# Kernel tuning notes

Measured on AMD Instinct MI355X. Metric: run time of the kernel, lower is better.

Reference implementation:

```python
import jax, jax.numpy as jnp
import numpy as np

P = 8.0  # Lp norm order for NormDist layers (finite-p distance conv)
CHUNK = 8  # output-channel chunk for memory-bounded distance computation
EPS = 8.0 / 255.0


def lp_norm(d, p=P):
    # stable Lp norm over last axis: m * (sum((d/m)^p))^(1/p)
    m = jnp.max(d, axis=-1)
    ms = jnp.where(m > 0, m, 1.0)
    s = jnp.sum((d / ms[..., None]) ** p, axis=-1)
    ss = jnp.where(m > 0, s, 1.0)
    return m * ss ** (1.0 / p)


def extract_patches(t, k, s, pad):
    # [B,C,H,W] -> [B, L, C*k*k] (torch-unfold channel-major ordering), L=Ho*Wo
    pt = jax.lax.conv_general_dilated_patches(t, (k, k), (s, s), [(pad, pad), (pad, pad)])
    B, F, Ho, Wo = pt.shape
    return pt.reshape(B, F, Ho * Wo).transpose(0, 2, 1), Ho, Wo


def normdist_conv(c, lo, hi, w, k, s, pad):
    # Lp-distance conv with interval bound propagation on (center, lower, upper)
    pc, Ho, Wo = extract_patches(c, k, s, pad)
    pl, _, _ = extract_patches(lo, k, s, pad)
    ph, _, _ = extract_patches(hi, k, s, pad)
    O = w.shape[0]
    wf = w.reshape(O, -1)  # [O, F]

    def per_chunk(wc):  # wc: [CHUNK, F]
        dc = jnp.abs(pc[:, :, None, :] - wc)                     # [B,L,CHUNK,F]
        oc = lp_norm(dc)
        # per-element distance bounds given lo <= x <= hi
        dl = jnp.maximum(jnp.maximum(pl[:, :, None, :] - wc, wc - ph[:, :, None, :]), 0.0)
        ol = lp_norm(dl)
        dh = jnp.maximum(jnp.abs(pl[:, :, None, :] - wc), jnp.abs(ph[:, :, None, :] - wc))
        oh = lp_norm(dh)
        return oc, ol, oh

    oc, ol, oh = jax.lax.map(per_chunk, wf.reshape(O // CHUNK, CHUNK, -1))

    def to_img(t):  # [nch, B, L, CHUNK] -> [B, O, Ho, Wo]
        nch, B, L, ch = t.shape
        return t.transpose(1, 0, 3, 2).reshape(B, nch * ch, Ho, Wo)

    return to_img(oc), to_img(ol), to_img(oh)


def bound_relu(c, lo, hi):
    return jax.nn.relu(c), jax.nn.relu(lo), jax.nn.relu(hi)


def _mp(t):
    return jax.lax.reduce_window(t, -jnp.inf, jax.lax.max, (1, 1, 3, 3), (1, 1, 2, 2), 'VALID')


def bound_maxpool(c, lo, hi):
    return _mp(c), _mp(lo), _mp(hi)


def bound_linear(c, lo, hi, W, b=None):
    oc = c @ W.T
    mid = ((lo + hi) * 0.5) @ W.T
    rad = ((hi - lo) * 0.5) @ jnp.abs(W).T
    if b is not None:
        oc = oc + b
        mid = mid + b
    return oc, mid - rad, mid + rad


def setup_inputs() -> dict:
    key = jax.random.key(0)
    ks = jax.random.split(key, 10)
    x = jax.random.normal(ks[0], (16, 3, 32, 32), jnp.float32)
    lower = x - EPS
    upper = x + EPS
    w1 = jax.random.normal(ks[1], (96, 3, 7, 7), jnp.float32)
    w2 = jax.random.normal(ks[2], (256, 96, 5, 5), jnp.float32)
    w3 = jax.random.normal(ks[3], (384, 256, 3, 3), jnp.float32)
    w4 = jax.random.normal(ks[4], (384, 384, 3, 3), jnp.float32)
    w5 = jax.random.normal(ks[5], (256, 384, 3, 3), jnp.float32)
    fw1 = jax.random.normal(ks[6], (1024, 2304), jnp.float32) * 0.02
    fw2 = jax.random.normal(ks[7], (512, 1024), jnp.float32) * 0.03
    fw3 = jax.random.normal(ks[8], (10, 512), jnp.float32) * 0.04
    fb3 = jax.random.normal(ks[9], (10,), jnp.float32)
    return {"x": x, "lower": lower, "upper": upper, "w1": w1, "w2": w2, "w3": w3,
            "w4": w4, "w5": w5, "fw1": fw1, "fw2": fw2, "fw3": fw3, "fb3": fb3}


def reference(x, lower, upper, w1, w2, w3, w4, w5, fw1, fw2, fw3, fb3):
    c, l, u = normdist_conv(x, lower, upper, w1, 7, 2, 2)   # 32 -> 15
    c, l, u = bound_relu(c, l, u)
    c, l, u = bound_maxpool(c, l, u)                        # 15 -> 7
    c, l, u = normdist_conv(c, l, u, w2, 5, 1, 2)           # 7 -> 7
    c, l, u = bound_relu(c, l, u)
    c, l, u = bound_maxpool(c, l, u)                        # 7 -> 3
    c, l, u = normdist_conv(c, l, u, w3, 3, 1, 1)
    c, l, u = bound_relu(c, l, u)
    c, l, u = normdist_conv(c, l, u, w4, 3, 1, 1)
    c, l, u = bound_relu(c, l, u)
    c, l, u = normdist_conv(c, l, u, w5, 3, 1, 1)
    c, l, u = bound_relu(c, l, u)
    B = c.shape[0]
    c, l, u = c.reshape(B, -1), l.reshape(B, -1), u.reshape(B, -1)
    c, l, u = bound_linear(c, l, u, fw1)
    c, l, u = bound_relu(c, l, u)
    c, l, u = bound_linear(c, l, u, fw2)
    c, l, u = bound_relu(c, l, u)
    c, l, u = bound_linear(c, l, u, fw3, fb3)
    # final negation swaps the roles of lower/upper
    return (-c, -u, -l)
```

## Files before the change

### kernel.cpp

```cpp
#include <hip/hip_runtime.h>
#include <math.h>


__device__ __forceinline__ float rt8(float s) { return sqrtf(sqrtf(sqrtf(s))); }

__device__ __forceinline__ void tap16(float w, float pc, float pl, float pu,
                                      float& aC, float& aL, float& aH)
{
    float a = pc - w; float a2 = a * a, a4 = a2 * a2; aC = fmaf(a4, a4, aC);
    float x = pl - w, y = pu - w;
    float dl = fmaxf(fmaxf(x, -y), 0.f);
    float e2 = dl * dl, e4 = e2 * e2; aL = fmaf(e4, e4, aL);
    float h2 = fmaxf(x * x, y * y);
    float h4 = h2 * h2; aH = fmaf(h4, h4, aH);
}

template<int K, int S, int PAD, int CC, int HIN, int WIN, int HO, int WO, bool ROOT>
__launch_bounds__(256)
__global__ void conv_a(const float* __restrict__ IC, const float* __restrict__ IL,
                       const float* __restrict__ IU, const float* __restrict__ W,
                       float* __restrict__ OUT, int B, int Cin, int O, int OG)
{
    constexpr int PH = (HO - 1) * S + K;
    constexpr int PW = (WO - 1) * S + K;
    constexpr int PP = PH * PW;
    constexpr int HW = HIN * WIN;
    constexpr int NP = HO * WO;
    constexpr int ROUNDS = (NP + 63) / 64;
    __shared__ float lds[CC * 3 * PP];

    int og = blockIdx.x % OG;
    int b  = (blockIdx.x / OG) % B;
    int chunk = blockIdx.x / (OG * B);
    int c0 = chunk * CC;
    int tid = threadIdx.x;

    for (int i = tid; i < CC * 3 * PP; i += 256) lds[i] = 0.f;
    __syncthreads();
    for (int tsel = 0; tsel < 3; ++tsel) {
        const float* src = (tsel == 0 ? IC : (tsel == 1 ? IL : IU))
                         + ((size_t)b * Cin + c0) * HW;
        for (int e = tid; e < CC * HW; e += 256) {
            int c = e / HW, p = e % HW;
            int pr = p / WIN, pw_ = p % WIN;
            lds[c * 3 * PP + tsel * PP + (pr + PAD) * PW + (pw_ + PAD)] = src[e];
        }
    }
    __syncthreads();

    int wave = tid >> 6, lane = tid & 63;
    int o = __builtin_amdgcn_readfirstlane(og * 4 + wave);
    const float* wp = W + ((size_t)o * Cin + c0) * (K * K);

    for (int r = 0; r < ROUNDS; ++r) {
        int pos = r * 64 + lane;
        bool act = pos < NP;
        int pp = act ? pos : 0;
        int oh = pp / WO, ow = pp % WO;
        const float* sl = lds + (oh * S) * PW + ow * S;
        const float* wc = wp;
        float aC = 0.f, aL = 0.f, aH = 0.f;
        for (int c = 0; c < CC; ++c) {
            #pragma unroll
            for (int kh = 0; kh < K; ++kh)
                #pragma unroll
                for (int kw = 0; kw < K; ++kw) {
                    float w = wc[kh * K + kw];
                    tap16(w, sl[kh * PW + kw], sl[PP + kh * PW + kw],
                          sl[2 * PP + kh * PW + kw], aC, aL, aH);
                }
            sl += 3 * PP; wc += K * K;
        }
        if (act) {
            size_t N = (size_t)B * O * NP;
            size_t oidx = ((size_t)b * O + o) * NP + pos;
            if (ROOT) {
                OUT[oidx] = rt8(aC); OUT[N + oidx] = rt8(aL); OUT[2 * N + oidx] = rt8(aH);
            } else {
                float* P = OUT + (size_t)chunk * 3 * N;
                P[oidx] = aC; P[N + oidx] = aL; P[2 * N + oidx] = aH;
            }
        }
    }
}

template<int CC>
__launch_bounds__(128)
__global__ void conv2_kernel(const float* __restrict__ IN, const float* __restrict__ W,
                             float* __restrict__ P, int nin)
{
    constexpr int B = 16, Cin = 96, O = 256;
    __shared__ float slab[CC * 165];
    int x = blockIdx.x;
    int pair = x % 2;
    int oh   = (x / 2) % 7;
    int b    = (x / 14) % B;
    int chunk = x / (14 * B);
    int c0 = chunk * CC;
    int tid = threadIdx.x;

    for (int i = tid; i < CC * 165; i += 128) {
        int c = i / 165; int rem = i % 165;
        int tsel = rem / 55; int rr = rem % 55;
        int r = rr / 11, col = rr % 11;
        int ih = oh + r - 2, iw = col - 2;
        float v = 0.f;
        if ((unsigned)ih < 7u && (unsigned)iw < 7u)
            v = IN[(size_t)tsel * nin + ((size_t)b * Cin + c0 + c) * 49 + ih * 7 + iw];
        slab[i] = v;
    }
    __syncthreads();

    int wave = tid >> 6, lane = tid & 63;
    int o = (pair * 2 + wave) * 64 + lane;

    float aC[7], aL[7], aH[7];
    #pragma unroll
    for (int u = 0; u < 7; ++u) { aC[u] = 0.f; aL[u] = 0.f; aH[u] = 0.f; }

    for (int c = 0; c < CC; ++c) {
        const float* wp = W + ((size_t)o * Cin + c0 + c) * 25;
        float w[25];
        #pragma unroll
        for (int t = 0; t < 25; ++t) w[t] = wp[t];
        const float* sb = slab + c * 165;
        #pragma unroll
        for (int r = 0; r < 5; ++r) {
            #pragma unroll
            for (int i = 0; i < 11; ++i) {
                float xc = sb[r * 11 + i];
                float xl = sb[55 + r * 11 + i];
                float xu = sb[110 + r * 11 + i];
                #pragma unroll
                for (int ow = 0; ow < 7; ++ow) {
                    int kw = i - ow;
                    if (kw >= 0 && kw < 5)
                        tap16(w[r * 5 + kw], xc, xl, xu, aC[ow], aL[ow], aH[ow]);
                }
            }
        }
    }

    size_t N = (size_t)B * O * 49;
    size_t base = (((size_t)b * O + o) * 7 + oh) * 7;
    float* Pc = P + (size_t)chunk * 3 * N;
    #pragma unroll
    for (int u = 0; u < 7; ++u) {
        Pc[base + u] = aC[u]; Pc[N + base + u] = aL[u]; Pc[2 * N + base + u] = aH[u];
    }
}

template<int CC>
__launch_bounds__(128)
__global__ void conv3x3_kernel(const float* __restrict__ IN, const float* __restrict__ W,
                               float* __restrict__ P, int nin, int B, int Cin, int O,
                               int PAIRS)
{
    __shared__ float slab[CC * 75];
    int x = blockIdx.x;
    int pair = x % PAIRS;
    int b    = (x / PAIRS) % B;
    int chunk = x / (PAIRS * B);
    int c0 = chunk * CC;
    int tid = threadIdx.x;

    for (int i = tid; i < CC * 75; i += 128) {
        int c = i / 75; int rem = i % 75;
        int tsel = rem / 25; int rr = rem % 25;
        int iy = rr / 5, ix = rr % 5;
        int ih = iy - 1, iw = ix - 1;
        float v = 0.f;
        if ((unsigned)ih < 3u && (unsigned)iw < 3u)
            v = IN[(size_t)tsel * nin + ((size_t)b * Cin + c0 + c) * 9 + ih * 3 + iw];
        slab[i] = v;
    }
    __syncthreads();

    int wave = tid >> 6, lane = tid & 63;
    int o = (pair * 2 + wave) * 64 + lane;

    float aC[9], aL[9], aH[9];
    #pragma unroll
    for (int u = 0; u < 9; ++u) { aC[u] = 0.f; aL[u] = 0.f; aH[u] = 0.f; }

    for (int c = 0; c < CC; ++c) {
        const float* wp = W + ((size_t)o * Cin + c0 + c) * 9;
        float w[9];
        #pragma unroll
        for (int t = 0; t < 9; ++t) w[t] = wp[t];
        const float* sb = slab + c * 75;
        #pragma unroll
        for (int iy = 0; iy < 5; ++iy) {
            #pragma unroll
            for (int ix = 0; ix < 5; ++ix) {
                float xc = sb[iy * 5 + ix];
                float xl = sb[25 + iy * 5 + ix];
                float xu = sb[50 + iy * 5 + ix];
                #pragma unroll
                for (int py = 0; py < 3; ++py) {
                    int ky = iy - py;
                    if (ky < 0 || ky > 2) continue;
                    #pragma unroll
                    for (int px = 0; px < 3; ++px) {
                        int kx = ix - px;
                        if (kx < 0 || kx > 2) continue;
                        tap16(w[ky * 3 + kx], xc, xl, xu,
                              aC[py * 3 + px], aL[py * 3 + px], aH[py * 3 + px]);
                    }
                }
            }
        }
    }

    size_t N = (size_t)B * O * 9;
    size_t base = ((size_t)b * O + o) * 9;
    float* Pc = P + (size_t)chunk * 3 * N;
    #pragma unroll
    for (int u = 0; u < 9; ++u) {
        Pc[base + u] = aC[u]; Pc[N + base + u] = aL[u]; Pc[2 * N + base + u] = aH[u];
    }
}

__global__ void conv_combine(const float* __restrict__ P, float* __restrict__ OUT,
                             size_t N, int NCH)
{
    size_t idx = (size_t)blockIdx.x * blockDim.x + threadIdx.x;
    if (idx >= 3 * N) return;
    float s = 0.f;
    for (int ch = 0; ch < NCH; ++ch) s += P[(size_t)ch * 3 * N + idx];
    OUT[idx] = rt8(s);
}

__global__ void maxpool_kernel(const float* __restrict__ in, float* __restrict__ out,
                               int BC, int Hin, int Win, int Ho, int Wo,
                               int n_in, int n_out)
{
    int idx = blockIdx.x * blockDim.x + threadIdx.x;
    int per = BC * Ho * Wo;
    if (idx >= 3 * per) return;
    int tsel = idx / per; int r = idx - tsel * per;
    int ow = r % Wo; int t2 = r / Wo;
    int oh = t2 % Ho; int bc = t2 / Ho;
    const float* ip = in + (size_t)tsel * n_in + (size_t)bc * Hin * Win;
    int ih0 = oh * 2, iw0 = ow * 2;
    float m = -INFINITY;
    #pragma unroll
    for (int i = 0; i < 3; ++i)
        #pragma unroll
        for (int j = 0; j < 3; ++j)
            m = fmaxf(m, ip[(ih0 + i) * Win + (iw0 + j)]);
    out[(size_t)tsel * n_out + r] = m;
}

__global__ void fc_partial(
    const float* __restrict__ IC, const float* __restrict__ IL, const float* __restrict__ IU,
    const float* __restrict__ W, float* __restrict__ P,
    int B, int In, int Out, int CC, int NCH)
{
    int idx = blockIdx.x * blockDim.x + threadIdx.x;
    if (idx >= NCH * B * Out) return;
    int o = idx % Out; int t = idx / Out;
    int b = t % B; int chunk = t / B;
    int i0 = chunk * CC;
    const float4* wr = (const float4*)(W  + (size_t)o * In + i0);
    const float4* cr = (const float4*)(IC + (size_t)b * In + i0);
    const float4* lr = (const float4*)(IL + (size_t)b * In + i0);
    const float4* ur = (const float4*)(IU + (size_t)b * In + i0);
    float sc = 0.f, sm = 0.f, sr = 0.f;
    for (int i = 0; i < CC / 4; ++i) {
        float4 w4 = wr[i], c4 = cr[i], l4 = lr[i], u4 = ur[i];
        sc = fmaf(c4.x, w4.x, sc); sc = fmaf(c4.y, w4.y, sc);
        sc = fmaf(c4.z, w4.z, sc); sc = fmaf(c4.w, w4.w, sc);
        sm = fmaf((l4.x + u4.x) * 0.5f, w4.x, sm);
        sm = fmaf((l4.y + u4.y) * 0.5f, w4.y, sm);
        sm = fmaf((l4.z + u4.z) * 0.5f, w4.z, sm);
        sm = fmaf((l4.w + u4.w) * 0.5f, w4.w, sm);
        sr = fmaf((u4.x - l4.x) * 0.5f, fabsf(w4.x), sr);
        sr = fmaf((u4.y - l4.y) * 0.5f, fabsf(w4.y), sr);
        sr = fmaf((u4.z - l4.z) * 0.5f, fabsf(w4.z), sr);
        sr = fmaf((u4.w - l4.w) * 0.5f, fabsf(w4.w), sr);
    }
    size_t N = (size_t)B * Out;
    size_t base = (size_t)b * Out + o;
    float* p = P + (size_t)chunk * 3 * N;
    p[base] = sc; p[N + base] = sm; p[2 * N + base] = sr;
}

__global__ void fc_combine(const float* __restrict__ P, float* __restrict__ OUT,
                           size_t N, int NCH)
{
    size_t idx = (size_t)blockIdx.x * blockDim.x + threadIdx.x;
    if (idx >= N) return;
    float sc = 0.f, sm = 0.f, sr = 0.f;
    for (int ch = 0; ch < NCH; ++ch) {
        const float* p = P + (size_t)ch * 3 * N;
        sc += p[idx]; sm += p[N + idx]; sr += p[2 * N + idx];
    }
    OUT[idx]         = fmaxf(sc, 0.f);
    OUT[N + idx]     = fmaxf(sm - sr, 0.f);
    OUT[2 * N + idx] = fmaxf(sm + sr, 0.f);
}

__global__ void bound_linear_kernel(
    const float* __restrict__ IC, const float* __restrict__ IL, const float* __restrict__ IU,
    const float* __restrict__ W, const float* __restrict__ bias,
    float* __restrict__ OC, float* __restrict__ OL, float* __restrict__ OU,
    int B, int In, int Out)
{
    int idx = blockIdx.x * blockDim.x + threadIdx.x;
    if (idx >= B * Out) return;
    int o = idx % Out, b = idx / Out;
    const float* wr = W  + (size_t)o * In;
    const float* cr = IC + (size_t)b * In;
    const float* lr = IL + (size_t)b * In;
    const float* ur = IU + (size_t)b * In;
    float sc = 0.f, sm = 0.f, sr = 0.f;
    for (int i = 0; i < In; ++i) {
        float w = wr[i];
        sc = fmaf(cr[i], w, sc);
        sm = fmaf((lr[i] + ur[i]) * 0.5f, w, sm);
        sr = fmaf((ur[i] - lr[i]) * 0.5f, fabsf(w), sr);
    }
    float bb = bias[o]; sc += bb; sm += bb;
    OC[idx] = -sc; OL[idx] = -(sm - sr); OU[idx] = -(sm + sr);
}

extern "C" void kernel_launch(void* const* d_in, const int* in_sizes, int n_in,
                              void* d_out, int out_size, void* d_ws, size_t ws_size,
                              hipStream_t stream)
{
    const float* x   = (const float*)d_in[0];
    const float* lo  = (const float*)d_in[1];
    const float* hi  = (const float*)d_in[2];
    const float* w1  = (const float*)d_in[3];
    const float* w2  = (const float*)d_in[4];
    const float* w3  = (const float*)d_in[5];
    const float* w4  = (const float*)d_in[6];
    const float* w5  = (const float*)d_in[7];
    const float* fw1 = (const float*)d_in[8];
    const float* fw2 = (const float*)d_in[9];
    const float* fw3 = (const float*)d_in[10];
    const float* fb3 = (const float*)d_in[11];
    float* out = (float*)d_out;
    float* ws  = (float*)d_ws;

    const size_t n_c1 = 16u * 96 * 15 * 15;
    const size_t n_p1 = 16u * 96 * 7 * 7;
    const size_t n_c2 = 16u * 256 * 7 * 7;
    const size_t n_p2 = 16u * 256 * 3 * 3;
    const size_t n_c3 = 16u * 384 * 3 * 3;
    const size_t n_c4 = n_c3;
    const size_t n_c5 = 16u * 256 * 3 * 3;
    const size_t n_f1 = 16u * 1024;
    const size_t n_f2 = 16u * 512;

    float* A  = ws;
    float* Bp = A  + 3 * n_c1;
    float* Cc = Bp + 3 * n_p1;
    float* D  = Cc + 3 * n_c2;
    float* E  = D  + 3 * n_p2;
    float* F  = E  + 3 * n_c3;
    float* G  = F  + 3 * n_c4;
    float* H  = G  + 3 * n_c5;
    float* I  = H  + 3 * n_f1;
    float* SP = I  + 3 * n_f2;

    const int BS = 256;
    auto grid = [](size_t tot) { return dim3((unsigned)((tot + 255) / 256)); };

    conv_a<7, 2, 2, 3, 32, 32, 15, 15, true><<<384, BS, 0, stream>>>(
        x, lo, hi, w1, A, 16, 3, 96, 24);
    maxpool_kernel<<<grid(3 * n_p1), BS, 0, stream>>>(
        A, Bp, 16 * 96, 15, 15, 7, 7, (int)n_c1, (int)n_p1);
    conv2_kernel<16><<<6 * 16 * 7 * 2, 128, 0, stream>>>(Bp, w2, SP, (int)n_p1);
    conv_combine<<<grid(3 * n_c2), BS, 0, stream>>>(SP, Cc, n_c2, 6);
    maxpool_kernel<<<grid(3 * n_p2), BS, 0, stream>>>(
        Cc, D, 16 * 256, 7, 7, 3, 3, (int)n_c2, (int)n_p2);
    conv3x3_kernel<8><<<32 * 16 * 3, 128, 0, stream>>>(
        D, w3, SP, (int)n_p2, 16, 256, 384, 3);
    conv_combine<<<grid(3 * n_c3), BS, 0, stream>>>(SP, E, n_c3, 32);
    conv3x3_kernel<12><<<32 * 16 * 3, 128, 0, stream>>>(
        E, w4, SP, (int)n_c3, 16, 384, 384, 3);
    conv_combine<<<grid(3 * n_c4), BS, 0, stream>>>(SP, F, n_c4, 32);
    conv3x3_kernel<12><<<32 * 16 * 2, 128, 0, stream>>>(
        F, w5, SP, (int)n_c4, 16, 384, 256, 2);
    conv_combine<<<grid(3 * n_c5), BS, 0, stream>>>(SP, G, n_c5, 32);
    fc_partial<<<grid(8u * 16 * 1024), BS, 0, stream>>>(
        G, G + n_c5, G + 2 * n_c5, fw1, SP, 16, 2304, 1024, 288, 8);
    fc_combine<<<grid(n_f1), BS, 0, stream>>>(SP, H, n_f1, 8);
    fc_partial<<<grid(8u * 16 * 512), BS, 0, stream>>>(
        H, H + n_f1, H + 2 * n_f1, fw2, SP, 16, 1024, 512, 128, 8);
    fc_combine<<<grid(n_f2), BS, 0, stream>>>(SP, I, n_f2, 8);
    bound_linear_kernel<<<grid(160), BS, 0, stream>>>(
        I, I + n_f2, I + 2 * n_f2, fw3, fb3,
        out, out + 320, out + 160, 16, 512, 10);
}
```

Before: 691.1 us.

## Transpose weights on device for coalesced loads and reshape conv grids

New measurement: 810.3 us. +17.2%, slower.

```diff
diff --git a/kernel.cpp b/kernel.cpp
--- a/kernel.cpp
+++ b/kernel.cpp
@@ -15,7 +15,15 @@
     float h4 = h2 * h2; aH = fmaf(h4, h4, aH);
 }
 
-template<int K, int S, int PAD, int CC, int HIN, int WIN, int HO, int WO, bool ROOT>
+__global__ void wtrans(const float* __restrict__ W, float* __restrict__ WT, int O, int CK)
+{
+    int idx = blockIdx.x * blockDim.x + threadIdx.x;
+    if (idx >= O * CK) return;
+    int o = idx % O, ck = idx / O;
+    WT[idx] = W[(size_t)o * CK + ck];
+}
+
+template<int K, int S, int PAD, int CC, int HIN, int WIN, int HO, int WO>
 __launch_bounds__(256)
 __global__ void conv_a(const float* __restrict__ IC, const float* __restrict__ IL,
                        const float* __restrict__ IU, const float* __restrict__ W,
@@ -31,15 +39,13 @@
 
     int og = blockIdx.x % OG;
     int b  = (blockIdx.x / OG) % B;
-    int chunk = blockIdx.x / (OG * B);
-    int c0 = chunk * CC;
     int tid = threadIdx.x;
 
     for (int i = tid; i < CC * 3 * PP; i += 256) lds[i] = 0.f;
     __syncthreads();
     for (int tsel = 0; tsel < 3; ++tsel) {
         const float* src = (tsel == 0 ? IC : (tsel == 1 ? IL : IU))
-                         + ((size_t)b * Cin + c0) * HW;
+                         + (size_t)b * Cin * HW;
         for (int e = tid; e < CC * HW; e += 256) {
             int c = e / HW, p = e % HW;
             int pr = p / WIN, pw_ = p % WIN;
@@ -50,7 +56,7 @@
 
     int wave = tid >> 6, lane = tid & 63;
     int o = __builtin_amdgcn_readfirstlane(og * 4 + wave);
-    const float* wp = W + ((size_t)o * Cin + c0) * (K * K);
+    const float* wp = W + (size_t)o * Cin * (K * K);
 
     for (int r = 0; r < ROUNDS; ++r) {
         int pos = r * 64 + lane;
@@ -74,35 +80,30 @@
         if (act) {
             size_t N = (size_t)B * O * NP;
             size_t oidx = ((size_t)b * O + o) * NP + pos;
-            if (ROOT) {
-                OUT[oidx] = rt8(aC); OUT[N + oidx] = rt8(aL); OUT[2 * N + oidx] = rt8(aH);
-            } else {
-                float* P = OUT + (size_t)chunk * 3 * N;
-                P[oidx] = aC; P[N + oidx] = aL; P[2 * N + oidx] = aH;
-            }
+            OUT[oidx] = rt8(aC); OUT[N + oidx] = rt8(aL); OUT[2 * N + oidx] = rt8(aH);
         }
     }
 }
 
 template<int CC>
-__launch_bounds__(128)
-__global__ void conv2_kernel(const float* __restrict__ IN, const float* __restrict__ W,
+__launch_bounds__(256)
+__global__ void conv2_kernel(const float* __restrict__ IN, const float* __restrict__ WT,
                              float* __restrict__ P, int nin)
 {
     constexpr int B = 16, Cin = 96, O = 256;
+    constexpr size_t N = (size_t)B * O * 49;
     __shared__ float slab[CC * 165];
     int x = blockIdx.x;
-    int pair = x % 2;
-    int oh   = (x / 2) % 7;
-    int b    = (x / 14) % B;
-    int chunk = x / (14 * B);
+    int oh   = x % 7;
+    int b    = (x / 7) % B;
+    int chunk = x / (7 * B);
     int c0 = chunk * CC;
     int tid = threadIdx.x;
 
-    for (int i = tid; i < CC * 165; i += 128) {
-        int c = i / 165; int rem = i % 165;
-        int tsel = rem / 55; int rr = rem % 55;
-        int r = rr / 11, col = rr % 11;
+    for (int i = tid; i < CC * 165; i += 256) {
+        int c = i / 165; int rem = i - c * 165;
+        int tsel = rem / 55; int rr = rem - tsel * 55;
+        int r = rr / 11, col = rr - r * 11;
         int ih = oh + r - 2, iw = col - 2;
         float v = 0.f;
         if ((unsigned)ih < 7u && (unsigned)iw < 7u)
@@ -111,18 +112,16 @@
     }
     __syncthreads();
 
-    int wave = tid >> 6, lane = tid & 63;
-    int o = (pair * 2 + wave) * 64 + lane;
-
+    int o = tid;
     float aC[7], aL[7], aH[7];
     #pragma unroll
     for (int u = 0; u < 7; ++u) { aC[u] = 0.f; aL[u] = 0.f; aH[u] = 0.f; }
 
     for (int c = 0; c < CC; ++c) {
-        const float* wp = W + ((size_t)o * Cin + c0 + c) * 25;
+        const float* wp = WT + (size_t)((c0 + c) * 25) * O + o;
         float w[25];
         #pragma unroll
-        for (int t = 0; t < 25; ++t) w[t] = wp[t];
+        for (int t = 0; t < 25; ++t) w[t] = wp[(size_t)t * O];
         const float* sb = slab + c * 165;
         #pragma unroll
         for (int r = 0; r < 5; ++r) {
@@ -141,33 +140,45 @@
         }
     }
 
-    size_t N = (size_t)B * O * 49;
-    size_t base = (((size_t)b * O + o) * 7 + oh) * 7;
     float* Pc = P + (size_t)chunk * 3 * N;
+    size_t rowbase = ((size_t)(b * 7 + oh) * 7) * O + o;
     #pragma unroll
     for (int u = 0; u < 7; ++u) {
-        Pc[base + u] = aC[u]; Pc[N + base + u] = aL[u]; Pc[2 * N + base + u] = aH[u];
-    }
+        Pc[rowbase + (size_t)u * O]         = aC[u];
+        Pc[N + rowbase + (size_t)u * O]     = aL[u];
+        Pc[2 * N + rowbase + (size_t)u * O] = aH[u];
+    }
+}
+
+__global__ void conv2_combine(const float* __restrict__ P, float* __restrict__ OUT, int NCH)
+{
+    constexpr int B = 16, O = 256;
+    constexpr size_t N = (size_t)B * O * 49;
+    size_t idx = (size_t)blockIdx.x * blockDim.x + threadIdx.x;
+    if (idx >= 3 * N) return;
+    float s = 0.f;
+    for (int ch = 0; ch < NCH; ++ch) s += P[(size_t)ch * 3 * N + idx];
+    size_t tsel = idx / N; size_t r = idx % N;
+    int o = (int)(r % O); int pos = (int)((r / O) % 49); int b = (int)(r / (O * 49));
+    OUT[tsel * N + ((size_t)b * O + o) * 49 + pos] = rt8(s);
 }
 
 template<int CC>
-__launch_bounds__(128)
-__global__ void conv3x3_kernel(const float* __restrict__ IN, const float* __restrict__ W,
-                               float* __restrict__ P, int nin, int B, int Cin, int O,
-                               int PAIRS)
+__launch_bounds__(384)
+__global__ void conv3x3_kernel(const float* __restrict__ IN, const float* __restrict__ WT,
+                               float* __restrict__ P, int nin, int B, int Cin, int O)
 {
     __shared__ float slab[CC * 75];
     int x = blockIdx.x;
-    int pair = x % PAIRS;
-    int b    = (x / PAIRS) % B;
-    int chunk = x / (PAIRS * B);
+    int b = x % B;
+    int chunk = x / B;
     int c0 = chunk * CC;
     int tid = threadIdx.x;
 
-    for (int i = tid; i < CC * 75; i += 128) {
-        int c = i / 75; int rem = i % 75;
-        int tsel = rem / 25; int rr = rem % 25;
-        int iy = rr / 5, ix = rr % 5;
+    for (int i = tid; i < CC * 75; i += blockDim.x) {
+        int c = i / 75; int rem = i - c * 75;
+        int tsel = rem / 25; int rr = rem - tsel * 25;
+        int iy = rr / 5, ix = rr - iy * 5;
         int ih = iy - 1, iw = ix - 1;
         float v = 0.f;
         if ((unsigned)ih < 3u && (unsigned)iw < 3u)
@@ -176,18 +187,16 @@
     }
     __syncthreads();
 
-    int wave = tid >> 6, lane = tid & 63;
-    int o = (pair * 2 + wave) * 64 + lane;
-
+    int o = tid;
     float aC[9], aL[9], aH[9];
     #pragma unroll
     for (int u = 0; u < 9; ++u) { aC[u] = 0.f; aL[u] = 0.f; aH[u] = 0.f; }
 
     for (int c = 0; c < CC; ++c) {
-        const float* wp = W + ((size_t)o * Cin + c0 + c) * 9;
+        const float* wp = WT + (size_t)((c0 + c) * 9) * O + o;
         float w[9];
         #pragma unroll
-        for (int t = 0; t < 9; ++t) w[t] = wp[t];
+        for (int t = 0; t < 9; ++t) w[t] = wp[(size_t)t * O];
         const float* sb = slab + c * 75;
         #pragma unroll
         for (int iy = 0; iy < 5; ++iy) {
@@ -213,22 +222,27 @@
     }
 
     size_t N = (size_t)B * O * 9;
-    size_t base = ((size_t)b * O + o) * 9;
     float* Pc = P + (size_t)chunk * 3 * N;
+    size_t base = ((size_t)b * 9) * O + o;
     #pragma unroll
     for (int u = 0; u < 9; ++u) {
-        Pc[base + u] = aC[u]; Pc[N + base + u] = aL[u]; Pc[2 * N + base + u] = aH[u];
-    }
-}
-
-__global__ void conv_combine(const float* __restrict__ P, float* __restrict__ OUT,
-                             size_t N, int NCH)
-{
+        Pc[base + (size_t)u * O]         = aC[u];
+        Pc[N + base + (size_t)u * O]     = aL[u];
+        Pc[2 * N + base + (size_t)u * O] = aH[u];
+    }
+}
+
+__global__ void conv3_combine(const float* __restrict__ P, float* __restrict__ OUT,
+                              int B, int O, int NCH)
+{
+    size_t N = (size_t)B * O * 9;
     size_t idx = (size_t)blockIdx.x * blockDim.x + threadIdx.x;
     if (idx >= 3 * N) return;
     float s = 0.f;
     for (int ch = 0; ch < NCH; ++ch) s += P[(size_t)ch * 3 * N + idx];
-    OUT[idx] = rt8(s);
+    size_t tsel = idx / N; size_t r = idx % N;
+    int o = (int)(r % O); int pos = (int)((r / O) % 9); int b = (int)(r / ((size_t)O * 9));
+    OUT[tsel * N + ((size_t)b * O + o) * 9 + pos] = rt8(s);
 }
 
 __global__ void maxpool_kernel(const float* __restrict__ in, float* __restrict__ out,
@@ -252,9 +266,9 @@
     out[(size_t)tsel * n_out + r] = m;
 }
 
-__global__ void fc_partial(
+__global__ void fc_partial_t(
     const float* __restrict__ IC, const float* __restrict__ IL, const float* __restrict__ IU,
-    const float* __restrict__ W, float* __restrict__ P,
+    const float* __restrict__ WT, float* __restrict__ P,
     int B, int In, int Out, int CC, int NCH)
 {
     int idx = blockIdx.x * blockDim.x + threadIdx.x;
@@ -262,23 +276,17 @@
     int o = idx % Out; int t = idx / Out;
     int b = t % B; int chunk = t / B;
     int i0 = chunk * CC;
-    const float4* wr = (const float4*)(W  + (size_t)o * In + i0);
-    const float4* cr = (const float4*)(IC + (size_t)b * In + i0);
-    const float4* lr = (const float4*)(IL + (size_t)b * In + i0);
-    const float4* ur = (const float4*)(IU + (size_t)b * In + i0);
+    const float* cr = IC + (size_t)b * In + i0;
+    const float* lr = IL + (size_t)b * In + i0;
+    const float* ur = IU + (size_t)b * In + i0;
+    const float* wp = WT + (size_t)i0 * Out + o;
     float sc = 0.f, sm = 0.f, sr = 0.f;
-    for (int i = 0; i < CC / 4; ++i) {
-        float4 w4 = wr[i], c4 = cr[i], l4 = lr[i], u4 = ur[i];
-        sc = fmaf(c4.x, w4.x, sc); sc = fmaf(c4.y, w4.y, sc);
-        sc = fmaf(c4.z, w4.z, sc); sc = fmaf(c4.w, w4.w, sc);
-        sm = fmaf((l4.x + u4.x) * 0.5f, w4.x, sm);
-        sm = fmaf((l4.y + u4.y) * 0.5f, w4.y, sm);
-        sm = fmaf((l4.z + u4.z) * 0.5f, w4.z, sm);
-        sm = fmaf((l4.w + u4.w) * 0.5f, w4.w, sm);
-        sr = fmaf((u4.x - l4.x) * 0.5f, fabsf(w4.x), sr);
-        sr = fmaf((u4.y - l4.y) * 0.5f, fabsf(w4.y), sr);
-        sr = fmaf((u4.z - l4.z) * 0.5f, fabsf(w4.z), sr);
-        sr = fmaf((u4.w - l4.w) * 0.5f, fabsf(w4.w), sr);
+    for (int i = 0; i < CC; ++i) {
+        float w = wp[(size_t)i * Out];
+        float c = cr[i], l = lr[i], u = ur[i];
+        sc = fmaf(c, w, sc);
+        sm = fmaf((l + u) * 0.5f, w, sm);
+        sr = fmaf((u - l) * 0.5f, fabsf(w), sr);
     }
     size_t N = (size_t)B * Out;
     size_t base = (size_t)b * Out + o;
@@ -354,42 +362,55 @@
     const size_t n_f1 = 16u * 1024;
     const size_t n_f2 = 16u * 512;
 
-    float* A  = ws;
-    float* Bp = A  + 3 * n_c1;
-    float* Cc = Bp + 3 * n_p1;
-    float* D  = Cc + 3 * n_c2;
-    float* E  = D  + 3 * n_p2;
-    float* F  = E  + 3 * n_c3;
-    float* G  = F  + 3 * n_c4;
-    float* H  = G  + 3 * n_c5;
-    float* I  = H  + 3 * n_f1;
-    float* SP = I  + 3 * n_f2;
+    float* A   = ws;
+    float* Bp  = A  + 3 * n_c1;
+    float* Cc  = Bp + 3 * n_p1;
+    float* D   = Cc + 3 * n_c2;
+    float* E   = D  + 3 * n_p2;
+    float* F   = E  + 3 * n_c3;
+    float* G   = F  + 3 * n_c4;
+    float* H   = G  + 3 * n_c5;
+    float* I   = H  + 3 * n_f1;
+    float* SP  = I  + 3 * n_f2;
+    float* WT2 = SP + 8000000;
+    float* WT3 = WT2 + 614400;
+    float* WT4 = WT3 + 884736;
+    float* WT5 = WT4 + 1327104;
+    float* WTF1 = SP + 1000000;
+    float* WTF2 = SP + 3500000;
 
     const int BS = 256;
     auto grid = [](size_t tot) { return dim3((unsigned)((tot + 255) / 256)); };
 
-    conv_a<7, 2, 2, 3, 32, 32, 15, 15, true><<<384, BS, 0, stream>>>(
+    wtrans<<<grid(614400),  BS, 0, stream>>>(w2, WT2, 256, 2400);
+    wtrans<<<grid(884736),  BS, 0, stream>>>(w3, WT3, 384, 2304);
+    wtrans<<<grid(1327104), BS, 0, stream>>>(w4, WT4, 384, 3456);
+    wtrans<<<grid(884736),  BS, 0, stream>>>(w5, WT5, 256, 3456);
+
+    conv_a<7, 2, 2, 3, 32, 32, 15, 15><<<384, BS, 0, stream>>>(
         x, lo, hi, w1, A, 16, 3, 96, 24);
     maxpool_kernel<<<grid(3 * n_p1), BS, 0, stream>>>(
         A, Bp, 16 * 96, 15, 15, 7, 7, (int)n_c1, (int)n_p1);
-    conv2_kernel<16><<<6 * 16 * 7 * 2, 128, 0, stream>>>(Bp, w2, SP, (int)n_p1);
-    conv_combine<<<grid(3 * n_c2), BS, 0, stream>>>(SP, Cc, n_c2, 6);
+    conv2_kernel<8><<<12 * 16 * 7, 256, 0, stream>>>(Bp, WT2, SP, (int)n_p1);
+    conv2_combine<<<grid(3 * n_c2), BS, 0, stream>>>(SP, Cc, 12);
     maxpool_kernel<<<grid(3 * n_p2), BS, 0, stream>>>(
         Cc, D, 16 * 256, 7, 7, 3, 3, (int)n_c2, (int)n_p2);
-    conv3x3_kernel<8><<<32 * 16 * 3, 128, 0, stream>>>(
-        D, w3, SP, (int)n_p2, 16, 256, 384, 3);
-    conv_combine<<<grid(3 * n_c3), BS, 0, stream>>>(SP, E, n_c3, 32);
-    conv3x3_kernel<12><<<32 * 16 * 3, 128, 0, stream>>>(
-        E, w4, SP, (int)n_c3, 16, 384, 384, 3);
-    conv_combine<<<grid(3 * n_c4), BS, 0, stream>>>(SP, F, n_c4, 32);
-    conv3x3_kernel<12><<<32 * 16 * 2, 128, 0, stream>>>(
-        F, w5, SP, (int)n_c4, 16, 384, 256, 2);
-    conv_combine<<<grid(3 * n_c5), BS, 0, stream>>>(SP, G, n_c5, 32);
-    fc_partial<<<grid(8u * 16 * 1024), BS, 0, stream>>>(
-        G, G + n_c5, G + 2 * n_c5, fw1, SP, 16, 2304, 1024, 288, 8);
+    conv3x3_kernel<8><<<32 * 16, 384, 0, stream>>>(
+        D, WT3, SP, (int)n_p2, 16, 256, 384);
+    conv3_combine<<<grid(3 * n_c3), BS, 0, stream>>>(SP, E, 16, 384, 32);
+    conv3x3_kernel<8><<<48 * 16, 384, 0, stream>>>(
+        E, WT4, SP, (int)n_c3, 16, 384, 384);
+    conv3_combine<<<grid(3 * n_c4), BS, 0, stream>>>(SP, F, 16, 384, 48);
+    conv3x3_kernel<8><<<48 * 16, 256, 0, stream>>>(
+        F, WT5, SP, (int)n_c4, 16, 384, 256);
+    conv3_combine<<<grid(3 * n_c5), BS, 0, stream>>>(SP, G, 16, 256, 48);
+    wtrans<<<grid(2359296), BS, 0, stream>>>(fw1, WTF1, 1024, 2304);
+    wtrans<<<grid(524288),  BS, 0, stream>>>(fw2, WTF2, 512, 1024);
+    fc_partial_t<<<grid(8u * 16 * 1024), BS, 0, stream>>>(
+        G, G + n_c5, G + 2 * n_c5, WTF1, SP, 16, 2304, 1024, 288, 8);
     fc_combine<<<grid(n_f1), BS, 0, stream>>>(SP, H, n_f1, 8);
-    fc_partial<<<grid(8u * 16 * 512), BS, 0, stream>>>(
-        H, H + n_f1, H + 2 * n_f1, fw2, SP, 16, 1024, 512, 128, 8);
+    fc_partial_t<<<grid(8u * 16 * 512), BS, 0, stream>>>(
+        H, H + n_f1, H + 2 * n_f1, WTF2, SP, 16, 1024, 512, 128, 8);
     fc_combine<<<grid(n_f2), BS, 0, stream>>>(SP, I, n_f2, 8);
     bound_linear_kernel<<<grid(160), BS, 0, stream>>>(
         I, I + n_f2, I + 2 * n_f2, fw3, fb3,
```
